# Optimization experiments

Hardware: AMD Instinct MI355X
Metric: run time of the kernel (lower is better)

The kernel has to match this reference:

```python
import jax, jax.numpy as jnp
import numpy as np

N_EMBD = 1024
N_HEAD = 16
HEAD_DIM = N_EMBD // N_HEAD
MASK_FILL = -10.0  # module uses -10, not -inf


def setup_inputs() -> dict:
    key = jax.random.key(0)
    kx, kq, kk, kv, ko = jax.random.split(key, 5)
    B, T = 4, 2048
    s = 1.0 / np.sqrt(N_EMBD)
    return {
        "x": jax.random.normal(kx, (B, T, N_EMBD), dtype=jnp.float32),
        "wq": jax.random.normal(kq, (N_EMBD, N_EMBD), dtype=jnp.float32) * s,
        "wk": jax.random.normal(kk, (N_EMBD, N_EMBD), dtype=jnp.float32) * s,
        "wv": jax.random.normal(kv, (N_EMBD, N_EMBD), dtype=jnp.float32) * s,
        "wo": jax.random.normal(ko, (N_EMBD, N_EMBD), dtype=jnp.float32) * s,
    }


def reference(x, wq, wk, wv, wo):
    B, T, C = x.shape
    # nn.Linear applies x @ W.T; weights here stored as [out, in]
    q = (x @ wq.T).reshape(B, T, N_HEAD, HEAD_DIM).transpose(0, 2, 1, 3)
    k = (x @ wk.T).reshape(B, T, N_HEAD, HEAD_DIM).transpose(0, 2, 1, 3)
    v = (x @ wv.T).reshape(B, T, N_HEAD, HEAD_DIM).transpose(0, 2, 1, 3)
    scale = 1.0 / np.sqrt(HEAD_DIM)
    att = jnp.einsum("bhqd,bhkd->bhqk", q, k) * scale  # [B,H,T,T]
    causal = jnp.tril(jnp.ones((T, T), dtype=bool))
    att = jnp.where(causal[None, None, :, :], att, MASK_FILL)
    att = jax.nn.softmax(att, axis=-1)
    y = jnp.einsum("bhqk,bhkd->bhqd", att, v)
    y = y.transpose(0, 2, 1, 3).reshape(B, T, C)
    return y @ wo.T
```

## Files before the change

kernel.cpp:

```cpp
#include <hip/hip_runtime.h>

typedef __attribute__((ext_vector_type(8))) short bf16x8;
typedef __attribute__((ext_vector_type(4))) float f32x4;

#define T_SEQ 2048
#define EXPM10 4.5399929762484854e-05f

#define WAIT_VM8 0xF78
#define WAIT_VM4 0xF74
#define WAIT_VM0 0xF70

__device__ __forceinline__ unsigned short f2bf(float f) {
    unsigned int u = __builtin_bit_cast(unsigned int, f);
    u += 0x7fffu + ((u >> 16) & 1u);
    return (unsigned short)(u >> 16);
}
__device__ __forceinline__ float bf2f(unsigned short u) {
    return __builtin_bit_cast(float, (unsigned int)u << 16);
}

__device__ __forceinline__ void async16(void* lds, const void* g) {
    __builtin_amdgcn_global_load_lds(
        (__attribute__((address_space(1))) void*)g,
        (__attribute__((address_space(3))) void*)lds, 16, 0, 0);
}

__global__ __launch_bounds__(256) void cvt_bf16(const float* __restrict__ src,
                                                unsigned short* __restrict__ dst, int n4) {
    int i = blockIdx.x * 256 + threadIdx.x;
    if (i < n4) {
        float4 v = ((const float4*)src)[i];
        ushort4 r;
        r.x = f2bf(v.x); r.y = f2bf(v.y); r.z = f2bf(v.z); r.w = f2bf(v.w);
        ((ushort4*)dst)[i] = r;
    }
}

__global__ __launch_bounds__(256) void cvt_w(const float* __restrict__ wq,
                                             const float* __restrict__ wk,
                                             const float* __restrict__ wv,
                                             const float* __restrict__ wo,
                                             unsigned short* __restrict__ wqkv,
                                             unsigned short* __restrict__ wob) {
    int which = blockIdx.x >> 10;
    int i = (blockIdx.x & 1023) * 256 + threadIdx.x;
    const float* src = which == 0 ? wq : which == 1 ? wk : which == 2 ? wv : wo;
    unsigned short* dst = which < 3 ? wqkv + (size_t)which * 1048576 : wob;
    float4 v = ((const float4*)src)[i];
    ushort4 r;
    r.x = f2bf(v.x); r.y = f2bf(v.y); r.z = f2bf(v.z); r.w = f2bf(v.w);
    ((ushort4*)dst)[i] = r;
}

__global__ __launch_bounds__(256) void gemm_qkv(const unsigned short* __restrict__ A,
                                                const unsigned short* __restrict__ B,
                                                unsigned short* __restrict__ Qb,
                                                unsigned short* __restrict__ Kb,
                                                unsigned short* __restrict__ Vtb) {
    __shared__ unsigned short As[3][4096];
    __shared__ unsigned short Bs[3][4096];
    const int K = 1024;
    int m0 = blockIdx.y * 128, n0 = blockIdx.x * 128;
    int tid = threadIdx.x;
    int wave = tid >> 6, lane = tid & 63;
    int r = lane & 15, q = lane >> 4;
    int wr = wave >> 1, wc = wave & 1;

    f32x4 acc[4][4];
#pragma unroll
    for (int i = 0; i < 4; i++)
#pragma unroll
        for (int j = 0; j < 4; j++) acc[i][j] = (f32x4){0.f, 0.f, 0.f, 0.f};

    int rw = tid >> 2, kc = (tid & 3) << 3;
    const unsigned short* a0 = A + (size_t)(m0 + rw) * K + kc;
    const unsigned short* a1 = A + (size_t)(m0 + 64 + rw) * K + kc;
    const unsigned short* b0 = B + (size_t)(n0 + rw) * K + kc;
    const unsigned short* b1 = B + (size_t)(n0 + 64 + rw) * K + kc;

    async16(&As[0][wave * 512], a0);
    async16(&As[0][2048 + wave * 512], a1);
    async16(&Bs[0][wave * 512], b0);
    async16(&Bs[0][2048 + wave * 512], b1);
    async16(&As[1][wave * 512], a0 + 32);
    async16(&As[1][2048 + wave * 512], a1 + 32);
    async16(&Bs[1][wave * 512], b0 + 32);
    async16(&Bs[1][2048 + wave * 512], b1 + 32);

    int cur = 0, pf = 2;
    for (int it = 0; it < 32; ++it) {
        __builtin_amdgcn_s_barrier();
        __builtin_amdgcn_sched_barrier(0);
        if (it + 2 < 32) {
            int ko = (it + 2) * 32;
            async16(&As[pf][wave * 512], a0 + ko);
            async16(&As[pf][2048 + wave * 512], a1 + ko);
            async16(&Bs[pf][wave * 512], b0 + ko);
            async16(&Bs[pf][2048 + wave * 512], b1 + ko);
            __builtin_amdgcn_sched_barrier(0);
            __builtin_amdgcn_s_waitcnt(WAIT_VM8);
        } else if (it + 1 < 32) {
            __builtin_amdgcn_s_waitcnt(WAIT_VM4);
        } else {
            __builtin_amdgcn_s_waitcnt(WAIT_VM0);
        }
        __builtin_amdgcn_s_barrier();
        __builtin_amdgcn_sched_barrier(0);

        bf16x8 af[4], bfr[4];
#pragma unroll
        for (int mi = 0; mi < 4; mi++)
            af[mi] = *(const bf16x8*)&As[cur][(wr * 64 + mi * 16 + r) * 32 + q * 8];
#pragma unroll
        for (int ni = 0; ni < 4; ni++)
            bfr[ni] = *(const bf16x8*)&Bs[cur][(wc * 64 + ni * 16 + r) * 32 + q * 8];
#pragma unroll
        for (int mi = 0; mi < 4; mi++)
#pragma unroll
            for (int ni = 0; ni < 4; ni++)
                acc[mi][ni] = __builtin_amdgcn_mfma_f32_16x16x32_bf16(
                    af[mi], bfr[ni], acc[mi][ni], 0, 0, 0);

        cur = cur == 2 ? 0 : cur + 1;
        pf = pf == 2 ? 0 : pf + 1;
    }

#pragma unroll
    for (int mi = 0; mi < 4; mi++) {
#pragma unroll
        for (int ni = 0; ni < 4; ni++) {
#pragma unroll
            for (int rr = 0; rr < 4; rr++) {
                int gm = m0 + wr * 64 + mi * 16 + q * 4 + rr;
                int gn = n0 + wc * 64 + ni * 16 + r;
                float v = acc[mi][ni][rr];
                int b = gm >> 11, t = gm & 2047;
                int sel = gn >> 10, nn = gn & 1023;
                int h = nn >> 6, d = nn & 63;
                if (sel == 0)
                    Qb[((size_t)(b * 16 + h) * 2048 + t) * 64 + d] = f2bf(v);
                else if (sel == 1)
                    Kb[((size_t)(b * 16 + h) * 2048 + t) * 64 + d] = f2bf(v);
                else
                    Vtb[((size_t)(b * 16 + h) * 64 + d) * 2048 + t] = f2bf(v);
            }
        }
    }
}

__global__ __launch_bounds__(256) void gemm_out(const unsigned short* __restrict__ A,
                                                const unsigned short* __restrict__ B,
                                                float* __restrict__ out) {
    __shared__ unsigned short As[3][4096];
    __shared__ unsigned short Bs[3][4096];
    const int K = 1024;
    int m0 = blockIdx.y * 128, n0 = blockIdx.x * 128;
    int tid = threadIdx.x;
    int wave = tid >> 6, lane = tid & 63;
    int r = lane & 15, q = lane >> 4;
    int wr = wave >> 1, wc = wave & 1;

    f32x4 acc[4][4];
#pragma unroll
    for (int i = 0; i < 4; i++)
#pragma unroll
        for (int j = 0; j < 4; j++) acc[i][j] = (f32x4){0.f, 0.f, 0.f, 0.f};

    int rw = tid >> 2, kc = (tid & 3) << 3;
    const unsigned short* a0 = A + (size_t)(m0 + rw) * K + kc;
    const unsigned short* a1 = A + (size_t)(m0 + 64 + rw) * K + kc;
    const unsigned short* b0 = B + (size_t)(n0 + rw) * K + kc;
    const unsigned short* b1 = B + (size_t)(n0 + 64 + rw) * K + kc;

    async16(&As[0][wave * 512], a0);
    async16(&As[0][2048 + wave * 512], a1);
    async16(&Bs[0][wave * 512], b0);
    async16(&Bs[0][2048 + wave * 512], b1);
    async16(&As[1][wave * 512], a0 + 32);
    async16(&As[1][2048 + wave * 512], a1 + 32);
    async16(&Bs[1][wave * 512], b0 + 32);
    async16(&Bs[1][2048 + wave * 512], b1 + 32);

    int cur = 0, pf = 2;
    for (int it = 0; it < 32; ++it) {
        __builtin_amdgcn_s_barrier();
        __builtin_amdgcn_sched_barrier(0);
        if (it + 2 < 32) {
            int ko = (it + 2) * 32;
            async16(&As[pf][wave * 512], a0 + ko);
            async16(&As[pf][2048 + wave * 512], a1 + ko);
            async16(&Bs[pf][wave * 512], b0 + ko);
            async16(&Bs[pf][2048 + wave * 512], b1 + ko);
            __builtin_amdgcn_sched_barrier(0);
            __builtin_amdgcn_s_waitcnt(WAIT_VM8);
        } else if (it + 1 < 32) {
            __builtin_amdgcn_s_waitcnt(WAIT_VM4);
        } else {
            __builtin_amdgcn_s_waitcnt(WAIT_VM0);
        }
        __builtin_amdgcn_s_barrier();
        __builtin_amdgcn_sched_barrier(0);

        bf16x8 af[4], bfr[4];
#pragma unroll
        for (int mi = 0; mi < 4; mi++)
            af[mi] = *(const bf16x8*)&As[cur][(wr * 64 + mi * 16 + r) * 32 + q * 8];
#pragma unroll
        for (int ni = 0; ni < 4; ni++)
            bfr[ni] = *(const bf16x8*)&Bs[cur][(wc * 64 + ni * 16 + r) * 32 + q * 8];
#pragma unroll
        for (int mi = 0; mi < 4; mi++)
#pragma unroll
            for (int ni = 0; ni < 4; ni++)
                acc[mi][ni] = __builtin_amdgcn_mfma_f32_16x16x32_bf16(
                    af[mi], bfr[ni], acc[mi][ni], 0, 0, 0);

        cur = cur == 2 ? 0 : cur + 1;
        pf = pf == 2 ? 0 : pf + 1;
    }

#pragma unroll
    for (int mi = 0; mi < 4; mi++)
#pragma unroll
        for (int ni = 0; ni < 4; ni++)
#pragma unroll
            for (int rr = 0; rr < 4; rr++) {
                int gm = m0 + wr * 64 + mi * 16 + q * 4 + rr;
                int gn = n0 + wc * 64 + ni * 16 + r;
                out[(size_t)gm * 1024 + gn] = acc[mi][ni][rr];
            }
}

__global__ __launch_bounds__(256) void suffix_sv(const unsigned short* __restrict__ Vt,
                                                 float* __restrict__ SV) {
    __shared__ float bsum[32][64];
    int bh = blockIdx.x;
    int d = threadIdx.x & 63, c = threadIdx.x >> 6;
    const unsigned short* base = Vt + ((size_t)bh * 64 + d) * T_SEQ;
#pragma unroll
    for (int jj = 0; jj < 8; jj++) {
        int j = c * 8 + jj;
        float s = 0.f;
#pragma unroll
        for (int t8 = 0; t8 < 8; t8++) {
            bf16x8 v = *(const bf16x8*)(base + j * 64 + t8 * 8);
#pragma unroll
            for (int e = 0; e < 8; e++) s += bf2f((unsigned short)v[e]);
        }
        bsum[j][d] = s;
    }
    __syncthreads();
    if (threadIdx.x < 64) {
        float run = 0.f;
        for (int j = 31; j >= 0; j--) {
            run += bsum[j][d];
            SV[((size_t)bh * 32 + j) * 64 + d] = run;
        }
    }
}

#define KST 72
#define VST 72
#define PST 72
__global__ __launch_bounds__(256) void attn(const unsigned short* __restrict__ Q,
                                            const unsigned short* __restrict__ Kg,
                                            const unsigned short* __restrict__ Vt,
                                            const float* __restrict__ SV,
                                            unsigned short* __restrict__ Y) {
    __shared__ unsigned short Ks[64 * KST];
    __shared__ unsigned short Vs[64 * VST];
    __shared__ unsigned short Ps[4][16 * PST];
    int bh = blockIdx.y;
    int tid = threadIdx.x, wave = tid >> 6, lane = tid & 63;
    int r = lane & 15, qd = lane >> 4;
    int b = bh >> 4, h = bh & 15;

    int srow = tid >> 2, scol = (tid & 3) * 16;
    const unsigned short* kg = Kg + ((size_t)bh * T_SEQ + srow) * 64 + scol;
    const unsigned short* vg = Vt + ((size_t)bh * 64 + srow) * T_SEQ + scol;
    const float scale = 0.125f;

#pragma unroll
    for (int phase = 0; phase < 2; phase++) {
        int qi = phase == 0 ? 16 + (int)blockIdx.x : 15 - (int)blockIdx.x;
        int q0 = qi * 64;
        int query = q0 + wave * 16 + r;

        const unsigned short* qptr = Q + ((size_t)bh * T_SEQ + query) * 64 + qd * 8;
        bf16x8 qf0 = *(const bf16x8*)qptr;
        bf16x8 qf1 = *(const bf16x8*)(qptr + 32);

        float l_lane = 0.0f;
        f32x4 o[4];
#pragma unroll
        for (int n = 0; n < 4; n++) o[n] = (f32x4){0.f, 0.f, 0.f, 0.f};

        bf16x8 pk0 = *(const bf16x8*)(kg);
        bf16x8 pk1 = *(const bf16x8*)(kg + 8);
        bf16x8 pv0 = *(const bf16x8*)(vg);
        bf16x8 pv1 = *(const bf16x8*)(vg + 8);

        int iters = qi + 1;
        for (int it = 0; it < iters; ++it) {
            __syncthreads();
            *(bf16x8*)&Ks[srow * KST + scol]     = pk0;
            *(bf16x8*)&Ks[srow * KST + scol + 8] = pk1;
            *(bf16x8*)&Vs[srow * VST + scol]     = pv0;
            *(bf16x8*)&Vs[srow * VST + scol + 8] = pv1;
            __syncthreads();
            if (it + 1 < iters) {
                size_t kn = (size_t)(it + 1) * 64;
                pk0 = *(const bf16x8*)(kg + kn * 64);
                pk1 = *(const bf16x8*)(kg + kn * 64 + 8);
                pv0 = *(const bf16x8*)(vg + kn);
                pv1 = *(const bf16x8*)(vg + kn + 8);
            }

            int k0 = it * 64;
            f32x4 st[4];
#pragma unroll
            for (int t = 0; t < 4; t++) {
                bf16x8 kf0 = *(const bf16x8*)&Ks[(t * 16 + r) * KST + qd * 8];
                bf16x8 kf1 = *(const bf16x8*)&Ks[(t * 16 + r) * KST + 32 + qd * 8];
                st[t] = (f32x4){0.f, 0.f, 0.f, 0.f};
                st[t] = __builtin_amdgcn_mfma_f32_16x16x32_bf16(kf0, qf0, st[t], 0, 0, 0);
                st[t] = __builtin_amdgcn_mfma_f32_16x16x32_bf16(kf1, qf1, st[t], 0, 0, 0);
            }

            float p[4][4], sum = 0.f;
            bool anymask = (k0 + 63 > q0 + wave * 16);
            if (anymask) {
#pragma unroll
                for (int t = 0; t < 4; t++)
#pragma unroll
                    for (int e = 0; e < 4; e++) {
                        int kgidx = k0 + t * 16 + qd * 4 + e;
                        float pe = __expf(st[t][e] * scale);
                        p[t][e] = (kgidx <= query) ? pe : EXPM10;
                        sum += p[t][e];
                    }
            } else {
#pragma unroll
                for (int t = 0; t < 4; t++)
#pragma unroll
                    for (int e = 0; e < 4; e++) {
                        p[t][e] = __expf(st[t][e] * scale);
                        sum += p[t][e];
                    }
            }
            l_lane += sum;

#pragma unroll
            for (int t = 0; t < 4; t++) {
                ushort4 pk;
                pk.x = f2bf(p[t][0]); pk.y = f2bf(p[t][1]);
                pk.z = f2bf(p[t][2]); pk.w = f2bf(p[t][3]);
                *(ushort4*)&Ps[wave][r * PST + t * 16 + qd * 4] = pk;
            }
            __builtin_amdgcn_sched_barrier(0);

            bf16x8 pf0 = *(const bf16x8*)&Ps[wave][r * PST + qd * 8];
            bf16x8 pf1 = *(const bf16x8*)&Ps[wave][r * PST + 32 + qd * 8];
#pragma unroll
            for (int n = 0; n < 4; n++) {
                bf16x8 vf0 = *(const bf16x8*)&Vs[(n * 16 + r) * VST + qd * 8];
                bf16x8 vf1 = *(const bf16x8*)&Vs[(n * 16 + r) * VST + 32 + qd * 8];
                o[n] = __builtin_amdgcn_mfma_f32_16x16x32_bf16(vf0, pf0, o[n], 0, 0, 0);
                o[n] = __builtin_amdgcn_mfma_f32_16x16x32_bf16(vf1, pf1, o[n], 0, 0, 0);
            }
        }

        float l_i = l_lane;
        l_i += __shfl_xor(l_i, 16);
        l_i += __shfl_xor(l_i, 32);

        int j = qi + 1;
        float pm = 0.f, tail_l = 0.f;
        float sv[4][4];
#pragma unroll
        for (int n = 0; n < 4; n++)
#pragma unroll
            for (int e = 0; e < 4; e++) sv[n][e] = 0.f;
        if (j < 32) {
            pm = EXPM10;
            tail_l = (float)(T_SEQ - 64 * j) * pm;
            const float* svp = SV + ((size_t)bh * 32 + j) * 64;
#pragma unroll
            for (int n = 0; n < 4; n++) {
                float4 f = *(const float4*)(svp + n * 16 + qd * 4);
                sv[n][0] = f.x; sv[n][1] = f.y; sv[n][2] = f.z; sv[n][3] = f.w;
            }
        }
        float inv = 1.0f / (l_i + tail_l);
#pragma unroll
        for (int n = 0; n < 4; n++) {
            ushort4 yk;
            yk.x = f2bf((o[n][0] + pm * sv[n][0]) * inv);
            yk.y = f2bf((o[n][1] + pm * sv[n][1]) * inv);
            yk.z = f2bf((o[n][2] + pm * sv[n][2]) * inv);
            yk.w = f2bf((o[n][3] + pm * sv[n][3]) * inv);
            *(ushort4*)&Y[(((size_t)b * T_SEQ + query) * 16 + h) * 64 + n * 16 + qd * 4] = yk;
        }
    }
}

extern "C" void kernel_launch(void* const* d_in, const int* in_sizes, int n_in,
                              void* d_out, int out_size, void* d_ws, size_t ws_size,
                              hipStream_t stream) {
    const float* x  = (const float*)d_in[0];
    const float* wq = (const float*)d_in[1];
    const float* wk = (const float*)d_in[2];
    const float* wv = (const float*)d_in[3];
    const float* wo = (const float*)d_in[4];

    char* ws = (char*)d_ws;
    const size_t MB = 1u << 20;
    unsigned short* xb   = (unsigned short*)(ws);
    unsigned short* Qb   = (unsigned short*)(ws + 16 * MB);
    unsigned short* Kb   = (unsigned short*)(ws + 32 * MB);
    unsigned short* Vtb  = (unsigned short*)(ws + 48 * MB);
    unsigned short* wqkv = (unsigned short*)(ws + 64 * MB);
    unsigned short* wob  = (unsigned short*)(ws + 70 * MB);
    unsigned short* Yb   = xb;
    float* SVf = (float*)d_out;

    cvt_bf16<<<8192, 256, 0, stream>>>(x, xb, 2097152);
    cvt_w<<<4096, 256, 0, stream>>>(wq, wk, wv, wo, wqkv, wob);

    gemm_qkv<<<dim3(24, 64), 256, 0, stream>>>(xb, wqkv, Qb, Kb, Vtb);

    suffix_sv<<<64, 256, 0, stream>>>(Vtb, SVf);

    attn<<<dim3(16, 64), 256, 0, stream>>>(Qb, Kb, Vtb, SVf, Yb);

    gemm_out<<<dim3(8, 64), 256, 0, stream>>>(Yb, wob, (float*)d_out);
}
```

Baseline: 292.9 us.

## Double-buffer K/V tiles in LDS, use exp2 and packed bf16 converts

Splits the K and V shared-memory tiles into two buffers. The next tile is written to LDS while the current one is consumed, which removes one __syncthreads per iteration and moves the register prefetch two tiles ahead. The scale is folded into a log2e constant so the softmax uses the native exp2 instruction, and the manual bf16 rounding is replaced with the hardware v_cvt_pk_bf16_f32 packed convert. The cost is doubled LDS for K/V, which may reduce occupancy, plus possible small rounding differences in the convert.

```diff
diff --git a/kernel.cpp b/kernel.cpp
--- a/kernel.cpp
+++ b/kernel.cpp
@@ -5,6 +5,7 @@
 
 #define T_SEQ 2048
 #define EXPM10 4.5399929762484854e-05f
+#define SCALE_LOG2E 0.18033688011112042f
 
 #define WAIT_VM8 0xF78
 #define WAIT_VM4 0xF74
@@ -267,8 +268,8 @@
                                             const unsigned short* __restrict__ Vt,
                                             const float* __restrict__ SV,
                                             unsigned short* __restrict__ Y) {
-    __shared__ unsigned short Ks[64 * KST];
-    __shared__ unsigned short Vs[64 * VST];
+    __shared__ unsigned short Ks[2][64 * KST];
+    __shared__ unsigned short Vs[2][64 * VST];
     __shared__ unsigned short Ps[4][16 * PST];
     int bh = blockIdx.y;
     int tid = threadIdx.x, wave = tid >> 6, lane = tid & 63;
@@ -278,7 +279,6 @@
     int srow = tid >> 2, scol = (tid & 3) * 16;
     const unsigned short* kg = Kg + ((size_t)bh * T_SEQ + srow) * 64 + scol;
     const unsigned short* vg = Vt + ((size_t)bh * 64 + srow) * T_SEQ + scol;
-    const float scale = 0.125f;
 
 #pragma unroll
     for (int phase = 0; phase < 2; phase++) {
@@ -295,33 +295,48 @@
 #pragma unroll
         for (int n = 0; n < 4; n++) o[n] = (f32x4){0.f, 0.f, 0.f, 0.f};
 
+        int iters = qi + 1;
+
         bf16x8 pk0 = *(const bf16x8*)(kg);
         bf16x8 pk1 = *(const bf16x8*)(kg + 8);
         bf16x8 pv0 = *(const bf16x8*)(vg);
         bf16x8 pv1 = *(const bf16x8*)(vg + 8);
-
-        int iters = qi + 1;
+        __syncthreads();
+        *(bf16x8*)&Ks[0][srow * KST + scol]     = pk0;
+        *(bf16x8*)&Ks[0][srow * KST + scol + 8] = pk1;
+        *(bf16x8*)&Vs[0][srow * VST + scol]     = pv0;
+        *(bf16x8*)&Vs[0][srow * VST + scol + 8] = pv1;
+        if (iters > 1) {
+            pk0 = *(const bf16x8*)(kg + 4096);
+            pk1 = *(const bf16x8*)(kg + 4096 + 8);
+            pv0 = *(const bf16x8*)(vg + 64);
+            pv1 = *(const bf16x8*)(vg + 64 + 8);
+        }
+
         for (int it = 0; it < iters; ++it) {
             __syncthreads();
-            *(bf16x8*)&Ks[srow * KST + scol]     = pk0;
-            *(bf16x8*)&Ks[srow * KST + scol + 8] = pk1;
-            *(bf16x8*)&Vs[srow * VST + scol]     = pv0;
-            *(bf16x8*)&Vs[srow * VST + scol + 8] = pv1;
-            __syncthreads();
             if (it + 1 < iters) {
-                size_t kn = (size_t)(it + 1) * 64;
-                pk0 = *(const bf16x8*)(kg + kn * 64);
-                pk1 = *(const bf16x8*)(kg + kn * 64 + 8);
-                pv0 = *(const bf16x8*)(vg + kn);
-                pv1 = *(const bf16x8*)(vg + kn + 8);
-            }
-
+                int nb = (it + 1) & 1;
+                *(bf16x8*)&Ks[nb][srow * KST + scol]     = pk0;
+                *(bf16x8*)&Ks[nb][srow * KST + scol + 8] = pk1;
+                *(bf16x8*)&Vs[nb][srow * VST + scol]     = pv0;
+                *(bf16x8*)&Vs[nb][srow * VST + scol + 8] = pv1;
+                if (it + 2 < iters) {
+                    size_t kn = (size_t)(it + 2) * 64;
+                    pk0 = *(const bf16x8*)(kg + kn * 64);
+                    pk1 = *(const bf16x8*)(kg + kn * 64 + 8);
+                    pv0 = *(const bf16x8*)(vg + kn);
+                    pv1 = *(const bf16x8*)(vg + kn + 8);
+                }
+            }
+
+            int bc = it & 1;
             int k0 = it * 64;
             f32x4 st[4];
 #pragma unroll
             for (int t = 0; t < 4; t++) {
-                bf16x8 kf0 = *(const bf16x8*)&Ks[(t * 16 + r) * KST + qd * 8];
-                bf16x8 kf1 = *(const bf16x8*)&Ks[(t * 16 + r) * KST + 32 + qd * 8];
+                bf16x8 kf0 = *(const bf16x8*)&Ks[bc][(t * 16 + r) * KST + qd * 8];
+                bf16x8 kf1 = *(const bf16x8*)&Ks[bc][(t * 16 + r) * KST + 32 + qd * 8];
                 st[t] = (f32x4){0.f, 0.f, 0.f, 0.f};
                 st[t] = __builtin_amdgcn_mfma_f32_16x16x32_bf16(kf0, qf0, st[t], 0, 0, 0);
                 st[t] = __builtin_amdgcn_mfma_f32_16x16x32_bf16(kf1, qf1, st[t], 0, 0, 0);
@@ -335,7 +350,7 @@
 #pragma unroll
                     for (int e = 0; e < 4; e++) {
                         int kgidx = k0 + t * 16 + qd * 4 + e;
-                        float pe = __expf(st[t][e] * scale);
+                        float pe = __builtin_amdgcn_exp2f(st[t][e] * SCALE_LOG2E);
                         p[t][e] = (kgidx <= query) ? pe : EXPM10;
                         sum += p[t][e];
                     }
@@ -344,7 +359,7 @@
                 for (int t = 0; t < 4; t++)
 #pragma unroll
                     for (int e = 0; e < 4; e++) {
-                        p[t][e] = __expf(st[t][e] * scale);
+                        p[t][e] = __builtin_amdgcn_exp2f(st[t][e] * SCALE_LOG2E);
                         sum += p[t][e];
                     }
             }
@@ -352,10 +367,11 @@
 
 #pragma unroll
             for (int t = 0; t < 4; t++) {
-                ushort4 pk;
-                pk.x = f2bf(p[t][0]); pk.y = f2bf(p[t][1]);
-                pk.z = f2bf(p[t][2]); pk.w = f2bf(p[t][3]);
-                *(ushort4*)&Ps[wave][r * PST + t * 16 + qd * 4] = pk;
+                unsigned int w0, w1;
+                asm("v_cvt_pk_bf16_f32 %0, %1, %2" : "=v"(w0) : "v"(p[t][0]), "v"(p[t][1]));
+                asm("v_cvt_pk_bf16_f32 %0, %1, %2" : "=v"(w1) : "v"(p[t][2]), "v"(p[t][3]));
+                uint2 w; w.x = w0; w.y = w1;
+                *(uint2*)&Ps[wave][r * PST + t * 16 + qd * 4] = w;
             }
             __builtin_amdgcn_sched_barrier(0);
 
@@ -363,8 +379,8 @@
             bf16x8 pf1 = *(const bf16x8*)&Ps[wave][r * PST + 32 + qd * 8];
 #pragma unroll
             for (int n = 0; n < 4; n++) {
-                bf16x8 vf0 = *(const bf16x8*)&Vs[(n * 16 + r) * VST + qd * 8];
-                bf16x8 vf1 = *(const bf16x8*)&Vs[(n * 16 + r) * VST + 32 + qd * 8];
+                bf16x8 vf0 = *(const bf16x8*)&Vs[bc][(n * 16 + r) * VST + qd * 8];
+                bf16x8 vf1 = *(const bf16x8*)&Vs[bc][(n * 16 + r) * VST + 32 + qd * 8];
                 o[n] = __builtin_amdgcn_mfma_f32_16x16x32_bf16(vf0, pf0, o[n], 0, 0, 0);
                 o[n] = __builtin_amdgcn_mfma_f32_16x16x32_bf16(vf1, pf1, o[n], 0, 0, 0);
             }
@@ -394,12 +410,15 @@
         float inv = 1.0f / (l_i + tail_l);
 #pragma unroll
         for (int n = 0; n < 4; n++) {
-            ushort4 yk;
-            yk.x = f2bf((o[n][0] + pm * sv[n][0]) * inv);
-            yk.y = f2bf((o[n][1] + pm * sv[n][1]) * inv);
-            yk.z = f2bf((o[n][2] + pm * sv[n][2]) * inv);
-            yk.w = f2bf((o[n][3] + pm * sv[n][3]) * inv);
-            *(ushort4*)&Y[(((size_t)b * T_SEQ + query) * 16 + h) * 64 + n * 16 + qd * 4] = yk;
+            float y0 = (o[n][0] + pm * sv[n][0]) * inv;
+            float y1 = (o[n][1] + pm * sv[n][1]) * inv;
+            float y2 = (o[n][2] + pm * sv[n][2]) * inv;
+            float y3 = (o[n][3] + pm * sv[n][3]) * inv;
+            unsigned int w0, w1;
+            asm("v_cvt_pk_bf16_f32 %0, %1, %2" : "=v"(w0) : "v"(y0), "v"(y1));
+            asm("v_cvt_pk_bf16_f32 %0, %1, %2" : "=v"(w1) : "v"(y2), "v"(y3));
+            uint2 w; w.x = w0; w.y = w1;
+            *(uint2*)&Y[(((size_t)b * T_SEQ + query) * 16 + h) * 64 + n * 16 + qd * 4] = w;
         }
     }
 }
```

Measured after the change: 304.4 us. 1.04x slower.
